# Optimization experiments

Hardware: AMD Instinct MI355X
Metric: run time of the kernel (lower is better)

Reference implementation:

```python
import jax, jax.numpy as jnp
import numpy as np

D_MODEL = 1024
HEADS = 16
HEAD_DIM = D_MODEL // HEADS


def setup_inputs() -> dict:
    key = jax.random.key(0)
    ks = jax.random.split(key, 11)
    B, S = 2, 2048
    scale = 1.0 / np.sqrt(D_MODEL)
    inp = {
        "Q": jax.random.normal(ks[0], (B, S, D_MODEL), jnp.float32),
        "K": jax.random.normal(ks[1], (B, S, D_MODEL), jnp.float32),
        "V": jax.random.normal(ks[2], (B, S, D_MODEL), jnp.float32),
        "Wq": jax.random.normal(ks[3], (D_MODEL, D_MODEL), jnp.float32) * scale,
        "bq": jnp.zeros((D_MODEL,), jnp.float32),
        "Wk": jax.random.normal(ks[4], (D_MODEL, D_MODEL), jnp.float32) * scale,
        "bk": jnp.zeros((D_MODEL,), jnp.float32),
        "Wv": jax.random.normal(ks[5], (D_MODEL, D_MODEL), jnp.float32) * scale,
        "bv": jnp.zeros((D_MODEL,), jnp.float32),
        "Wo": jax.random.normal(ks[6], (D_MODEL, D_MODEL), jnp.float32) * scale,
        "bo": jnp.zeros((D_MODEL,), jnp.float32),
    }
    return inp


def reference(Q, K, V, Wq, bq, Wk, bk, Wv, bv, Wo, bo):
    B, S, _ = Q.shape
    # Linear projections (nn.Linear: x @ W^T + b), split into heads: [B, H, S, Dh]
    def proj(x, W, b):
        y = x @ W.T + b
        return y.reshape(B, S, HEADS, HEAD_DIM).transpose(0, 2, 1, 3)

    q = proj(Q, Wq, bq)
    k = proj(K, Wk, bk)
    v = proj(V, Wv, bv)

    # Scaled dot-product attention (dropout is identity in eval / p=0)
    scores = jnp.einsum("bhqd,bhkd->bhqk", q, k) / jnp.sqrt(
        jnp.asarray(HEAD_DIM, q.dtype)
    )
    weights = jax.nn.softmax(scores, axis=-1)
    ctx = jnp.einsum("bhqk,bhkd->bhqd", weights, v)  # [B, H, S, Dh]

    # Concatenate heads and output projection
    concat = ctx.transpose(0, 2, 1, 3).reshape(B, S, D_MODEL)
    return concat @ Wo.T + bo
```

## Files before the change

kernel.cpp:

```cpp
#include <hip/hip_runtime.h>
#include <hip/hip_bf16.h>

#define D_MODEL 1024
#define HEADS 16
#define HDIM 64
#define BATCH 2
#define SEQ 2048
#define MROWS (BATCH*SEQ)

typedef __attribute__((ext_vector_type(8))) short bf16x8;
typedef __attribute__((ext_vector_type(4))) float f32x4;
typedef __attribute__((ext_vector_type(16))) float f32x16;
typedef __attribute__((ext_vector_type(4))) float float4v;
typedef __attribute__((ext_vector_type(4))) unsigned u32x4;
typedef __attribute__((ext_vector_type(4))) short s16x4;

typedef const __attribute__((address_space(1))) void gconst_t;
typedef __attribute__((address_space(3))) void lds_t;
#define GLD16(g, l) __builtin_amdgcn_global_load_lds((gconst_t*)(g), (lds_t*)(l), 16, 0, 0)

#if __has_builtin(__builtin_amdgcn_exp2f)
#define EXP2(x) __builtin_amdgcn_exp2f(x)
#else
#define EXP2(x) __builtin_exp2f(x)
#endif

__device__ __forceinline__ unsigned short f2b(float f) {
  unsigned u = __builtin_bit_cast(unsigned, f);
  u += 0x7fffu + ((u >> 16) & 1u);
  return (unsigned short)(u >> 16);
}

__device__ __forceinline__ unsigned cvtpk(float lo, float hi) {
  unsigned r;
  asm volatile("v_cvt_pk_bf16_f32 %0, %1, %2" : "=v"(r) : "v"(lo), "v"(hi));
  return r;
}

__global__ __launch_bounds__(256)
void cast_all(const float* __restrict__ Q, const float* __restrict__ K,
              const float* __restrict__ V, const float* __restrict__ Wq,
              const float* __restrict__ Wk, const float* __restrict__ Wv,
              const float* __restrict__ Wo, char* __restrict__ ws)
{
  const size_t MB = 1024*1024;
  int b = blockIdx.x;
  const float* src; short* dst; int rb;
  if (b < 6144) {
    int t = b >> 11; rb = b & 2047;
    src = (t == 0) ? Q : (t == 1) ? K : V;
    dst = (short*)(ws + (size_t)t*8*MB);
  } else {
    int t = (b - 6144) >> 9; rb = (b - 6144) & 511;
    src = (t == 0) ? Wq : (t == 1) ? Wk : (t == 2) ? Wv : Wo;
    dst = (short*)(ws + (24 + 2*(size_t)t)*MB);
  }
  int i = rb*256 + threadIdx.x;
  const float4v* s = (const float4v*)src;
  float4v a = s[2*(size_t)i], c = s[2*(size_t)i + 1];
  bf16x8 o;
  o[0] = (short)f2b(a[0]); o[1] = (short)f2b(a[1]);
  o[2] = (short)f2b(a[2]); o[3] = (short)f2b(a[3]);
  o[4] = (short)f2b(c[0]); o[5] = (short)f2b(c[1]);
  o[6] = (short)f2b(c[2]); o[7] = (short)f2b(c[3]);
  *(bf16x8*)(dst + 8*(size_t)i) = o;
}

__global__ __launch_bounds__(256)
void gemm_qkv(const short* __restrict__ Qb, const short* __restrict__ Kb,
              const short* __restrict__ Vb, const short* __restrict__ Wqb,
              const short* __restrict__ Wkb, const short* __restrict__ Wvb,
              const float* __restrict__ bq, const float* __restrict__ bk,
              const float* __restrict__ bv, short* __restrict__ qp,
              short* __restrict__ kp, short* __restrict__ vp)
{
  __shared__ __align__(16) char smemc[65536];
  short* const lA0 = (short*)smemc;
  short* const lA1 = (short*)(smemc + 16384);
  short* const lB0 = (short*)(smemc + 32768);
  short* const lB1 = (short*)(smemc + 49152);
  short* const lT  = (short*)smemc;

  const int z = blockIdx.z;
  const short* A = (z == 0) ? Qb : (z == 1) ? Kb : Vb;
  const short* W = (z == 0) ? Wqb : (z == 1) ? Wkb : Wvb;
  const float* bias = (z == 0) ? bq : (z == 1) ? bk : bv;

  const int tid  = threadIdx.x;
  const int wid  = tid >> 6;
  const int lane = tid & 63;
  const int bm = blockIdx.x, bn = blockIdx.y;
  const int wr = wid >> 1, wc = wid & 1;

  f32x4 acc[4][4] = {};

  const int srow = tid >> 3;
  const int cswz = (((tid & 7) * 16) ^ ((srow & 7) << 4)) >> 1;
  const short* gA = A + (size_t)(bm*128 + srow)*D_MODEL + cswz;
  const short* gB = W + (size_t)(bn*128 + srow)*D_MODEL + cswz;

#define QKV_STAGE(kt, bA, bB) do { \
    const int ko_ = (kt)*64; \
    GLD16(gA + ko_,              (bA) + (     wid*8)*64); \
    GLD16(gA + 32*D_MODEL + ko_, (bA) + (32 + wid*8)*64); \
    GLD16(gA + 64*D_MODEL + ko_, (bA) + (64 + wid*8)*64); \
    GLD16(gA + 96*D_MODEL + ko_, (bA) + (96 + wid*8)*64); \
    GLD16(gB + ko_,              (bB) + (     wid*8)*64); \
    GLD16(gB + 32*D_MODEL + ko_, (bB) + (32 + wid*8)*64); \
    GLD16(gB + 64*D_MODEL + ko_, (bB) + (64 + wid*8)*64); \
    GLD16(gB + 96*D_MODEL + ko_, (bB) + (96 + wid*8)*64); \
  } while (0)

  const int fro = lane & 15;
  const int xr7 = (fro & 7) << 4;
  const int c0  = ((((lane >> 4) << 4))      ^ xr7) >> 1;
  const int c1  = ((64 + ((lane >> 4) << 4)) ^ xr7) >> 1;

  QKV_STAGE(0, lA0, lB0);
  __syncthreads();

  for (int kt = 0; kt < D_MODEL/64; ++kt) {
    const int cur = kt & 1;
    if (kt + 1 < D_MODEL/64)
      QKV_STAGE(kt + 1, cur ? lA0 : lA1, cur ? lB0 : lB1);
    const short* LA = cur ? lA1 : lA0;
    const short* LB = cur ? lB1 : lB0;
    #pragma unroll
    for (int ks2 = 0; ks2 < 2; ++ks2) {
      const int cc = ks2 ? c1 : c0;
      bf16x8 af[4], bfv[4];
      #pragma unroll
      for (int i = 0; i < 4; ++i)
        af[i] = *(const bf16x8*)&LA[(wr*64 + i*16 + fro)*64 + cc];
      #pragma unroll
      for (int j = 0; j < 4; ++j)
        bfv[j] = *(const bf16x8*)&LB[(wc*64 + j*16 + fro)*64 + cc];
      #pragma unroll
      for (int i = 0; i < 4; ++i)
        #pragma unroll
        for (int j = 0; j < 4; ++j)
          acc[i][j] = __builtin_amdgcn_mfma_f32_16x16x32_bf16(af[i], bfv[j], acc[i][j], 0, 0, 0);
    }
    __syncthreads();
  }
#undef QKV_STAGE

  if (z < 2) {
    const float sc = (z == 0) ? 0.125f*1.44269504f : 1.0f;
    short* out = (z == 0) ? qp : kp;
    #pragma unroll
    for (int i = 0; i < 4; ++i) {
      #pragma unroll
      for (int r = 0; r < 4; ++r) {
        const int m = bm*128 + wr*64 + i*16 + (lane>>4)*4 + r;
        const int b = m >> 11, s = m & (SEQ-1);
        #pragma unroll
        for (int j = 0; j < 4; ++j) {
          const int n = bn*128 + wc*64 + j*16 + fro;
          const int h = n >> 6, dh = n & 63;
          float v = (acc[i][j][r] + bias[n]) * sc;
          out[((size_t)(b*HEADS + h)*SEQ + s)*HDIM + dh] = (short)f2b(v);
        }
      }
    }
  } else {
    #pragma unroll
    for (int i = 0; i < 4; ++i) {
      #pragma unroll
      for (int r = 0; r < 4; ++r) {
        const int ml = wr*64 + i*16 + (lane>>4)*4 + r;
        #pragma unroll
        for (int j = 0; j < 4; ++j) {
          const int nl = wc*64 + j*16 + fro;
          lT[nl*129 + ml] = (short)f2b(acc[i][j][r] + bias[bn*128 + nl]);
        }
      }
    }
    __syncthreads();
    const int nl = tid >> 1, mh = (tid & 1) * 64;
    const int n = bn*128 + nl, h = n >> 6, dh = n & 63;
    const int b  = (bm*128) >> 11;
    const int s0 = (bm*128) & (SEQ-1);
    const size_t base = ((size_t)(b*HEADS + h)*HDIM + dh)*SEQ + s0 + mh;
    #pragma unroll
    for (int v8 = 0; v8 < 8; ++v8) {
      bf16x8 vv;
      #pragma unroll
      for (int e = 0; e < 8; ++e) vv[e] = lT[nl*129 + mh + v8*8 + e];
      *(bf16x8*)&vp[base + v8*8] = vv;
    }
  }
}

__global__ __launch_bounds__(256)
void gemm_out(const short* __restrict__ A, const short* __restrict__ W,
              const float* __restrict__ bias, float* __restrict__ out)
{
  __shared__ __align__(16) char smemc[65536];
  short* const lA0 = (short*)smemc;
  short* const lA1 = (short*)(smemc + 16384);
  short* const lB0 = (short*)(smemc + 32768);
  short* const lB1 = (short*)(smemc + 49152);

  const int tid  = threadIdx.x;
  const int wid  = tid >> 6;
  const int lane = tid & 63;
  const int bm = blockIdx.x, bn = blockIdx.y;
  const int wr = wid >> 1, wc = wid & 1;

  f32x4 acc[4][4] = {};
  const int srow = tid >> 3;
  const int cswz = (((tid & 7) * 16) ^ ((srow & 7) << 4)) >> 1;
  const short* gA = A + (size_t)(bm*128 + srow)*D_MODEL + cswz;
  const short* gB = W + (size_t)(bn*128 + srow)*D_MODEL + cswz;

#define OUT_STAGE(kt, bA, bB) do { \
    const int ko_ = (kt)*64; \
    GLD16(gA + ko_,              (bA) + (     wid*8)*64); \
    GLD16(gA + 32*D_MODEL + ko_, (bA) + (32 + wid*8)*64); \
    GLD16(gA + 64*D_MODEL + ko_, (bA) + (64 + wid*8)*64); \
    GLD16(gA + 96*D_MODEL + ko_, (bA) + (96 + wid*8)*64); \
    GLD16(gB + ko_,              (bB) + (     wid*8)*64); \
    GLD16(gB + 32*D_MODEL + ko_, (bB) + (32 + wid*8)*64); \
    GLD16(gB + 64*D_MODEL + ko_, (bB) + (64 + wid*8)*64); \
    GLD16(gB + 96*D_MODEL + ko_, (bB) + (96 + wid*8)*64); \
  } while (0)

  const int fro = lane & 15;
  const int xr7 = (fro & 7) << 4;
  const int c0  = ((((lane >> 4) << 4))      ^ xr7) >> 1;
  const int c1  = ((64 + ((lane >> 4) << 4)) ^ xr7) >> 1;

  OUT_STAGE(0, lA0, lB0);
  __syncthreads();

  for (int kt = 0; kt < D_MODEL/64; ++kt) {
    const int cur = kt & 1;
    if (kt + 1 < D_MODEL/64)
      OUT_STAGE(kt + 1, cur ? lA0 : lA1, cur ? lB0 : lB1);
    const short* LA = cur ? lA1 : lA0;
    const short* LB = cur ? lB1 : lB0;
    #pragma unroll
    for (int ks2 = 0; ks2 < 2; ++ks2) {
      const int cc = ks2 ? c1 : c0;
      bf16x8 af[4], bfv[4];
      #pragma unroll
      for (int i = 0; i < 4; ++i)
        af[i] = *(const bf16x8*)&LA[(wr*64 + i*16 + fro)*64 + cc];
      #pragma unroll
      for (int j = 0; j < 4; ++j)
        bfv[j] = *(const bf16x8*)&LB[(wc*64 + j*16 + fro)*64 + cc];
      #pragma unroll
      for (int i = 0; i < 4; ++i)
        #pragma unroll
        for (int j = 0; j < 4; ++j)
          acc[i][j] = __builtin_amdgcn_mfma_f32_16x16x32_bf16(af[i], bfv[j], acc[i][j], 0, 0, 0);
    }
    __syncthreads();
  }
#undef OUT_STAGE

  #pragma unroll
  for (int i = 0; i < 4; ++i) {
    #pragma unroll
    for (int r = 0; r < 4; ++r) {
      const int m = bm*128 + wr*64 + i*16 + (lane>>4)*4 + r;
      #pragma unroll
      for (int j = 0; j < 4; ++j) {
        const int n = bn*128 + wc*64 + j*16 + fro;
        out[(size_t)m*D_MODEL + n] = acc[i][j][r] + bias[n];
      }
    }
  }
}

__global__ __launch_bounds__(512)
void attn(const short* __restrict__ qws, const short* __restrict__ kws,
          const short* __restrict__ vws, short* __restrict__ ctx)
{
  __shared__ __align__(16) short lK[2][2][64*64];
  __shared__ __align__(16) short lV[2][2][64*64];

  const int tid = threadIdx.x, wid = tid >> 6, lane = tid & 63;
  const int sw = wid & 3, half = wid >> 2;
  const int bid = blockIdx.x;
  const int wg = (bid & 7) * 64 + (bid >> 3);
  const int qt = wg & 15, bh = wg >> 4;
  const size_t hb = (size_t)bh * SEQ * HDIM;

  const int lane31 = lane & 31, hi = lane >> 5;
  const int tidl = sw*64 + lane;
  const int tr0  = tidl >> 3;
  const int cswz = (((tidl & 7) * 16) ^ ((tr0 & 7) << 4)) >> 1;

  const short* gK = kws + hb;
  const short* gV = vws + hb;

#define STAGEKV(t, bb) do { \
    GLD16(gK + (size_t)((t)*64 + tr0)*HDIM + cswz,      &lK[half][bb][(sw*8)*64]); \
    GLD16(gK + (size_t)((t)*64 + 32 + tr0)*HDIM + cswz, &lK[half][bb][(32+sw*8)*64]); \
    GLD16(gV + (size_t)tr0*SEQ + (t)*64 + cswz,         &lV[half][bb][(sw*8)*64]); \
    GLD16(gV + (size_t)(32+tr0)*SEQ + (t)*64 + cswz,    &lV[half][bb][(32+sw*8)*64]); \
  } while (0)

  const int kt0 = half * 16;
  STAGEKV(kt0, 0);

  const int q = qt*128 + sw*32 + lane31;
  const short* gq = qws + hb + (size_t)q*HDIM + hi*8;
  bf16x8 qf[4];
  #pragma unroll
  for (int ks = 0; ks < 4; ++ks) qf[ks] = *(const bf16x8*)(gq + ks*16);

  f32x16 o0 = {}, o1 = {};
  float lrow = 0.f;
  const int swz = (lane31 & 7) << 4;

  __syncthreads();

  for (int k2 = 0; k2 < 16; ++k2) {
    const short* Kc = &lK[half][k2 & 1][0];
    const short* Vc = &lV[half][k2 & 1][0];
    if (k2 + 1 < 16) STAGEKV(kt0 + k2 + 1, (k2 + 1) & 1);

    #pragma unroll
    for (int kb = 0; kb < 2; ++kb) {
      f32x16 s = {};
      __builtin_amdgcn_s_setprio(1);
      #pragma unroll
      for (int ks = 0; ks < 4; ++ks) {
        bf16x8 kf = *(const bf16x8*)&Kc[(kb*32 + lane31)*64 + (((ks*32 + hi*16) ^ swz) >> 1)];
        s = __builtin_amdgcn_mfma_f32_32x32x16_bf16(kf, qf[ks], s, 0, 0, 0);
      }
      __builtin_amdgcn_s_setprio(0);

      float p[16]; float rs = 0.f;
      #pragma unroll
      for (int r = 0; r < 16; ++r) { p[r] = EXP2(s[r]); rs += p[r]; }
      lrow += rs;

      unsigned w0 = cvtpk(p[0],  p[1]),  w1 = cvtpk(p[2],  p[3]);
      unsigned w2 = cvtpk(p[4],  p[5]),  w3 = cvtpk(p[6],  p[7]);
      unsigned w4 = cvtpk(p[8],  p[9]),  w5 = cvtpk(p[10], p[11]);
      unsigned w6 = cvtpk(p[12], p[13]), w7 = cvtpk(p[14], p[15]);
      unsigned y0 = hi ? w0 : w2, y1 = hi ? w1 : w3;
      unsigned y2 = hi ? w4 : w6, y3 = hi ? w5 : w7;
      unsigned z0 = (unsigned)__shfl_xor((int)y0, 32);
      unsigned z1 = (unsigned)__shfl_xor((int)y1, 32);
      unsigned z2 = (unsigned)__shfl_xor((int)y2, 32);
      unsigned z3 = (unsigned)__shfl_xor((int)y3, 32);
      u32x4 pw0 = { hi ? z0 : w0, hi ? z1 : w1, hi ? w2 : z0, hi ? w3 : z1 };
      u32x4 pw1 = { hi ? z2 : w4, hi ? z3 : w5, hi ? w6 : z2, hi ? w7 : z3 };
      bf16x8 pa0 = __builtin_bit_cast(bf16x8, pw0);
      bf16x8 pa1 = __builtin_bit_cast(bf16x8, pw1);

      __builtin_amdgcn_s_setprio(1);
      #pragma unroll
      for (int ksl = 0; ksl < 2; ++ksl) {
        const int vcol = ((kb*64 + ksl*32 + hi*16) ^ swz) >> 1;
        bf16x8 pav = ksl ? pa1 : pa0;
        bf16x8 vf0 = *(const bf16x8*)&Vc[lane31*64 + vcol];
        bf16x8 vf1 = *(const bf16x8*)&Vc[(32 + lane31)*64 + vcol];
        o0 = __builtin_amdgcn_mfma_f32_32x32x16_bf16(vf0, pav, o0, 0, 0, 0);
        o1 = __builtin_amdgcn_mfma_f32_32x32x16_bf16(vf1, pav, o1, 0, 0, 0);
      }
      __builtin_amdgcn_s_setprio(0);
    }
    __syncthreads();
  }

  lrow += __shfl_xor(lrow, 32);

  float* xo = (float*)&lK[0][0][0];
  float* xl = (float*)&lV[0][0][0];
  if (half == 1) {
    #pragma unroll
    for (int g = 0; g < 4; ++g) {
      #pragma unroll
      for (int e = 0; e < 4; ++e) {
        const int dh = g*8 + hi*4 + e;
        xo[sw*2048 + dh*32 + lane31]        = o0[g*4 + e];
        xo[sw*2048 + (32 + dh)*32 + lane31] = o1[g*4 + e];
      }
    }
    if (hi == 0) xl[sw*32 + lane31] = lrow;
  }
  __syncthreads();
  if (half == 0) {
    const float inv = 1.0f / (lrow + xl[sw*32 + lane31]);
    const int b_ = bh >> 4, h_ = bh & (HEADS-1);
    const size_t base = ((size_t)(b_*SEQ) + q)*D_MODEL + h_*HDIM;
    #pragma unroll
    for (int g = 0; g < 4; ++g) {
      s16x4 pk0, pk1;
      #pragma unroll
      for (int e = 0; e < 4; ++e) {
        const int dh = g*8 + hi*4 + e;
        pk0[e] = (short)f2b((o0[g*4+e] + xo[sw*2048 + dh*32 + lane31]) * inv);
        pk1[e] = (short)f2b((o1[g*4+e] + xo[sw*2048 + (32+dh)*32 + lane31]) * inv);
      }
      *(s16x4*)&ctx[base +      g*8 + hi*4] = pk0;
      *(s16x4*)&ctx[base + 32 + g*8 + hi*4] = pk1;
    }
  }
#undef STAGEKV
}

extern "C" void kernel_launch(void* const* d_in, const int* in_sizes, int n_in,
                              void* d_out, int out_size, void* d_ws, size_t ws_size,
                              hipStream_t stream)
{
  const float* Q  = (const float*)d_in[0];
  const float* K  = (const float*)d_in[1];
  const float* V  = (const float*)d_in[2];
  const float* Wq = (const float*)d_in[3];
  const float* bq = (const float*)d_in[4];
  const float* Wk = (const float*)d_in[5];
  const float* bk = (const float*)d_in[6];
  const float* Wv = (const float*)d_in[7];
  const float* bv = (const float*)d_in[8];
  const float* Wo = (const float*)d_in[9];
  const float* bo = (const float*)d_in[10];

  char* ws = (char*)d_ws;
  const size_t MB = 1024*1024;
  short* Qb  = (short*)(ws +  0*MB);
  short* Kb  = (short*)(ws +  8*MB);
  short* Vb  = (short*)(ws + 16*MB);
  short* Wqb = (short*)(ws + 24*MB);
  short* Wkb = (short*)(ws + 26*MB);
  short* Wvb = (short*)(ws + 28*MB);
  short* Wob = (short*)(ws + 30*MB);
  short* qp  = (short*)(ws + 32*MB);
  short* kp  = (short*)(ws + 40*MB);
  short* vp  = (short*)(ws + 48*MB);
  short* cx  = (short*)(ws + 56*MB);

  cast_all<<<8192, 256, 0, stream>>>(Q, K, V, Wq, Wk, Wv, Wo, ws);
  gemm_qkv<<<dim3(MROWS/128, D_MODEL/128, 3), 256, 0, stream>>>(
      Qb, Kb, Vb, Wqb, Wkb, Wvb, bq, bk, bv, qp, kp, vp);
  attn<<<512, 512, 0, stream>>>(qp, kp, vp, cx);
  gemm_out<<<dim3(MROWS/128, D_MODEL/128), 256, 0, stream>>>(cx, Wob, bo, (float*)d_out);
}
```

Before: 118.8 us.

## Fuse fp32-to-bf16 cast into GEMM tile loads, drop separate cast kernel

Removes the standalone cast_all kernel and has gemm_qkv and gemm_out read fp32 inputs and weights directly. Each thread loads them into registers, converts with v_cvt_pk_bf16_f32, and writes the swizzled bf16 tile to LDS after the MFMA loop, giving register-staged double buffering. This cuts a kernel launch and the write-then-reread of the bf16 copies. In exchange the GEMMs read twice as many bytes per tile, re-read each weight fp32 tile from many blocks, and use more registers.

```diff
diff --git a/kernel.cpp b/kernel.cpp
--- a/kernel.cpp
+++ b/kernel.cpp
@@ -37,39 +37,16 @@
   return r;
 }
 
+__device__ __forceinline__ bf16x8 cvt8(float4v lo, float4v hi) {
+  u32x4 u = { cvtpk(lo[0], lo[1]), cvtpk(lo[2], lo[3]),
+              cvtpk(hi[0], hi[1]), cvtpk(hi[2], hi[3]) };
+  return __builtin_bit_cast(bf16x8, u);
+}
+
 __global__ __launch_bounds__(256)
-void cast_all(const float* __restrict__ Q, const float* __restrict__ K,
-              const float* __restrict__ V, const float* __restrict__ Wq,
-              const float* __restrict__ Wk, const float* __restrict__ Wv,
-              const float* __restrict__ Wo, char* __restrict__ ws)
-{
-  const size_t MB = 1024*1024;
-  int b = blockIdx.x;
-  const float* src; short* dst; int rb;
-  if (b < 6144) {
-    int t = b >> 11; rb = b & 2047;
-    src = (t == 0) ? Q : (t == 1) ? K : V;
-    dst = (short*)(ws + (size_t)t*8*MB);
-  } else {
-    int t = (b - 6144) >> 9; rb = (b - 6144) & 511;
-    src = (t == 0) ? Wq : (t == 1) ? Wk : (t == 2) ? Wv : Wo;
-    dst = (short*)(ws + (24 + 2*(size_t)t)*MB);
-  }
-  int i = rb*256 + threadIdx.x;
-  const float4v* s = (const float4v*)src;
-  float4v a = s[2*(size_t)i], c = s[2*(size_t)i + 1];
-  bf16x8 o;
-  o[0] = (short)f2b(a[0]); o[1] = (short)f2b(a[1]);
-  o[2] = (short)f2b(a[2]); o[3] = (short)f2b(a[3]);
-  o[4] = (short)f2b(c[0]); o[5] = (short)f2b(c[1]);
-  o[6] = (short)f2b(c[2]); o[7] = (short)f2b(c[3]);
-  *(bf16x8*)(dst + 8*(size_t)i) = o;
-}
-
-__global__ __launch_bounds__(256)
-void gemm_qkv(const short* __restrict__ Qb, const short* __restrict__ Kb,
-              const short* __restrict__ Vb, const short* __restrict__ Wqb,
-              const short* __restrict__ Wkb, const short* __restrict__ Wvb,
+void gemm_qkv(const float* __restrict__ Qf, const float* __restrict__ Kf,
+              const float* __restrict__ Vf, const float* __restrict__ Wqf,
+              const float* __restrict__ Wkf, const float* __restrict__ Wvf,
               const float* __restrict__ bq, const float* __restrict__ bk,
               const float* __restrict__ bv, short* __restrict__ qp,
               short* __restrict__ kp, short* __restrict__ vp)
@@ -82,8 +59,8 @@
   short* const lT  = (short*)smemc;
 
   const int z = blockIdx.z;
-  const short* A = (z == 0) ? Qb : (z == 1) ? Kb : Vb;
-  const short* W = (z == 0) ? Wqb : (z == 1) ? Wkb : Wvb;
+  const float* A = (z == 0) ? Qf : (z == 1) ? Kf : Vf;
+  const float* W = (z == 0) ? Wqf : (z == 1) ? Wkf : Wvf;
   const float* bias = (z == 0) ? bq : (z == 1) ? bk : bv;
 
   const int tid  = threadIdx.x;
@@ -95,34 +72,40 @@
   f32x4 acc[4][4] = {};
 
   const int srow = tid >> 3;
-  const int cswz = (((tid & 7) * 16) ^ ((srow & 7) << 4)) >> 1;
-  const short* gA = A + (size_t)(bm*128 + srow)*D_MODEL + cswz;
-  const short* gB = W + (size_t)(bn*128 + srow)*D_MODEL + cswz;
-
-#define QKV_STAGE(kt, bA, bB) do { \
-    const int ko_ = (kt)*64; \
-    GLD16(gA + ko_,              (bA) + (     wid*8)*64); \
-    GLD16(gA + 32*D_MODEL + ko_, (bA) + (32 + wid*8)*64); \
-    GLD16(gA + 64*D_MODEL + ko_, (bA) + (64 + wid*8)*64); \
-    GLD16(gA + 96*D_MODEL + ko_, (bA) + (96 + wid*8)*64); \
-    GLD16(gB + ko_,              (bB) + (     wid*8)*64); \
-    GLD16(gB + 32*D_MODEL + ko_, (bB) + (32 + wid*8)*64); \
-    GLD16(gB + 64*D_MODEL + ko_, (bB) + (64 + wid*8)*64); \
-    GLD16(gB + 96*D_MODEL + ko_, (bB) + (96 + wid*8)*64); \
-  } while (0)
+  const int gseg = (tid & 7) * 8;
+  const int dso  = ((((tid & 7) * 16) ^ ((srow & 7) << 4)) >> 1);
+  const float* gA = A + (size_t)(bm*128 + srow)*D_MODEL + gseg;
+  const float* gB = W + (size_t)(bn*128 + srow)*D_MODEL + gseg;
+
+  float4v sa[8], sb[8];
+#define QKV_LOAD(kt_) do { \
+    const int ko_ = (kt_)*64; \
+    _Pragma("unroll") \
+    for (int r_ = 0; r_ < 4; ++r_) { \
+      sa[2*r_]   = *(const float4v*)(gA + (size_t)r_*32*D_MODEL + ko_); \
+      sa[2*r_+1] = *(const float4v*)(gA + (size_t)r_*32*D_MODEL + ko_ + 4); \
+      sb[2*r_]   = *(const float4v*)(gB + (size_t)r_*32*D_MODEL + ko_); \
+      sb[2*r_+1] = *(const float4v*)(gB + (size_t)r_*32*D_MODEL + ko_ + 4); \
+    } } while (0)
+#define QKV_WRITE(bA_, bB_) do { \
+    _Pragma("unroll") \
+    for (int r_ = 0; r_ < 4; ++r_) { \
+      *(bf16x8*)&(bA_)[(32*r_ + srow)*64 + dso] = cvt8(sa[2*r_], sa[2*r_+1]); \
+      *(bf16x8*)&(bB_)[(32*r_ + srow)*64 + dso] = cvt8(sb[2*r_], sb[2*r_+1]); \
+    } } while (0)
 
   const int fro = lane & 15;
   const int xr7 = (fro & 7) << 4;
   const int c0  = ((((lane >> 4) << 4))      ^ xr7) >> 1;
   const int c1  = ((64 + ((lane >> 4) << 4)) ^ xr7) >> 1;
 
-  QKV_STAGE(0, lA0, lB0);
+  QKV_LOAD(0);
+  QKV_WRITE(lA0, lB0);
   __syncthreads();
 
   for (int kt = 0; kt < D_MODEL/64; ++kt) {
     const int cur = kt & 1;
-    if (kt + 1 < D_MODEL/64)
-      QKV_STAGE(kt + 1, cur ? lA0 : lA1, cur ? lB0 : lB1);
+    if (kt + 1 < D_MODEL/64) QKV_LOAD(kt + 1);
     const short* LA = cur ? lA1 : lA0;
     const short* LB = cur ? lB1 : lB0;
     #pragma unroll
@@ -141,9 +124,12 @@
         for (int j = 0; j < 4; ++j)
           acc[i][j] = __builtin_amdgcn_mfma_f32_16x16x32_bf16(af[i], bfv[j], acc[i][j], 0, 0, 0);
     }
+    if (kt + 1 < D_MODEL/64)
+      QKV_WRITE(cur ? lA0 : lA1, cur ? lB0 : lB1);
     __syncthreads();
   }
-#undef QKV_STAGE
+#undef QKV_LOAD
+#undef QKV_WRITE
 
   if (z < 2) {
     const float sc = (z == 0) ? 0.125f*1.44269504f : 1.0f;
@@ -193,7 +179,7 @@
 }
 
 __global__ __launch_bounds__(256)
-void gemm_out(const short* __restrict__ A, const short* __restrict__ W,
+void gemm_out(const short* __restrict__ A, const float* __restrict__ W,
               const float* __restrict__ bias, float* __restrict__ out)
 {
   __shared__ __align__(16) char smemc[65536];
@@ -210,20 +196,31 @@
 
   f32x4 acc[4][4] = {};
   const int srow = tid >> 3;
-  const int cswz = (((tid & 7) * 16) ^ ((srow & 7) << 4)) >> 1;
+  const int gseg = (tid & 7) * 8;
+  const int dso  = ((((tid & 7) * 16) ^ ((srow & 7) << 4)) >> 1);
+  const int cswz = dso;
   const short* gA = A + (size_t)(bm*128 + srow)*D_MODEL + cswz;
-  const short* gB = W + (size_t)(bn*128 + srow)*D_MODEL + cswz;
-
-#define OUT_STAGE(kt, bA, bB) do { \
-    const int ko_ = (kt)*64; \
-    GLD16(gA + ko_,              (bA) + (     wid*8)*64); \
-    GLD16(gA + 32*D_MODEL + ko_, (bA) + (32 + wid*8)*64); \
-    GLD16(gA + 64*D_MODEL + ko_, (bA) + (64 + wid*8)*64); \
-    GLD16(gA + 96*D_MODEL + ko_, (bA) + (96 + wid*8)*64); \
-    GLD16(gB + ko_,              (bB) + (     wid*8)*64); \
-    GLD16(gB + 32*D_MODEL + ko_, (bB) + (32 + wid*8)*64); \
-    GLD16(gB + 64*D_MODEL + ko_, (bB) + (64 + wid*8)*64); \
-    GLD16(gB + 96*D_MODEL + ko_, (bB) + (96 + wid*8)*64); \
+  const float* gB = W + (size_t)(bn*128 + srow)*D_MODEL + gseg;
+
+  float4v sb[8];
+#define OUT_LOADB(kt_) do { \
+    const int ko_ = (kt_)*64; \
+    _Pragma("unroll") \
+    for (int r_ = 0; r_ < 4; ++r_) { \
+      sb[2*r_]   = *(const float4v*)(gB + (size_t)r_*32*D_MODEL + ko_); \
+      sb[2*r_+1] = *(const float4v*)(gB + (size_t)r_*32*D_MODEL + ko_ + 4); \
+    } } while (0)
+#define OUT_WRITEB(bB_) do { \
+    _Pragma("unroll") \
+    for (int r_ = 0; r_ < 4; ++r_) \
+      *(bf16x8*)&(bB_)[(32*r_ + srow)*64 + dso] = cvt8(sb[2*r_], sb[2*r_+1]); \
+    } while (0)
+#define OUT_STAGEA(kt_, bA_) do { \
+    const int ko_ = (kt_)*64; \
+    GLD16(gA + ko_,              (bA_) + (     wid*8)*64); \
+    GLD16(gA + 32*D_MODEL + ko_, (bA_) + (32 + wid*8)*64); \
+    GLD16(gA + 64*D_MODEL + ko_, (bA_) + (64 + wid*8)*64); \
+    GLD16(gA + 96*D_MODEL + ko_, (bA_) + (96 + wid*8)*64); \
   } while (0)
 
   const int fro = lane & 15;
@@ -231,13 +228,17 @@
   const int c0  = ((((lane >> 4) << 4))      ^ xr7) >> 1;
   const int c1  = ((64 + ((lane >> 4) << 4)) ^ xr7) >> 1;
 
-  OUT_STAGE(0, lA0, lB0);
+  OUT_LOADB(0);
+  OUT_STAGEA(0, lA0);
+  OUT_WRITEB(lB0);
   __syncthreads();
 
   for (int kt = 0; kt < D_MODEL/64; ++kt) {
     const int cur = kt & 1;
-    if (kt + 1 < D_MODEL/64)
-      OUT_STAGE(kt + 1, cur ? lA0 : lA1, cur ? lB0 : lB1);
+    if (kt + 1 < D_MODEL/64) {
+      OUT_LOADB(kt + 1);
+      OUT_STAGEA(kt + 1, cur ? lA0 : lA1);
+    }
     const short* LA = cur ? lA1 : lA0;
     const short* LB = cur ? lB1 : lB0;
     #pragma unroll
@@ -256,9 +257,13 @@
         for (int j = 0; j < 4; ++j)
           acc[i][j] = __builtin_amdgcn_mfma_f32_16x16x32_bf16(af[i], bfv[j], acc[i][j], 0, 0, 0);
     }
+    if (kt + 1 < D_MODEL/64)
+      OUT_WRITEB(cur ? lB0 : lB1);
     __syncthreads();
   }
-#undef OUT_STAGE
+#undef OUT_LOADB
+#undef OUT_WRITEB
+#undef OUT_STAGEA
 
   #pragma unroll
   for (int i = 0; i < 4; ++i) {
@@ -424,21 +429,13 @@
 
   char* ws = (char*)d_ws;
   const size_t MB = 1024*1024;
-  short* Qb  = (short*)(ws +  0*MB);
-  short* Kb  = (short*)(ws +  8*MB);
-  short* Vb  = (short*)(ws + 16*MB);
-  short* Wqb = (short*)(ws + 24*MB);
-  short* Wkb = (short*)(ws + 26*MB);
-  short* Wvb = (short*)(ws + 28*MB);
-  short* Wob = (short*)(ws + 30*MB);
   short* qp  = (short*)(ws + 32*MB);
   short* kp  = (short*)(ws + 40*MB);
   short* vp  = (short*)(ws + 48*MB);
   short* cx  = (short*)(ws + 56*MB);
 
-  cast_all<<<8192, 256, 0, stream>>>(Q, K, V, Wq, Wk, Wv, Wo, ws);
   gemm_qkv<<<dim3(MROWS/128, D_MODEL/128, 3), 256, 0, stream>>>(
-      Qb, Kb, Vb, Wqb, Wkb, Wvb, bq, bk, bv, qp, kp, vp);
+      Q, K, V, Wq, Wk, Wv, bq, bk, bv, qp, kp, vp);
   attn<<<512, 512, 0, stream>>>(qp, kp, vp, cx);
-  gemm_out<<<dim3(MROWS/128, D_MODEL/128), 256, 0, stream>>>(cx, Wob, bo, (float*)d_out);
-}
+  gemm_out<<<dim3(MROWS/128, D_MODEL/128), 256, 0, stream>>>(cx, Wo, bo, (float*)d_out);
+}
```

Measured after the change: 124.7 us. 1.05x slower.

## Process two 32-query tiles per wave in attention, halving block size

Applied to the files above, without the earlier changes.

Each attention wave now handles 64 queries (two 32-row sub-tiles) instead of 32, so every K and V fragment read from LDS feeds two MFMAs. The block shrinks from 8 to 4 waves, and K/V staging is restructured so each wave issues 8 global-to-LDS loads instead of 4. This cuts LDS read traffic per FLOP and raises MFMA density per wave. In exchange it doubles accumulator and Q registers, which may reduce occupancy or cause spills, and leaves fewer waves to hide latency.

```diff
diff --git a/kernel.cpp b/kernel.cpp
--- a/kernel.cpp
+++ b/kernel.cpp
@@ -274,7 +274,7 @@
   }
 }
 
-__global__ __launch_bounds__(512)
+__global__ __launch_bounds__(256)
 void attn(const short* __restrict__ qws, const short* __restrict__ kws,
           const short* __restrict__ vws, short* __restrict__ ctx)
 {
@@ -282,38 +282,43 @@
   __shared__ __align__(16) short lV[2][2][64*64];
 
   const int tid = threadIdx.x, wid = tid >> 6, lane = tid & 63;
-  const int sw = wid & 3, half = wid >> 2;
+  const int half = wid >> 1, sq = wid & 1;
   const int bid = blockIdx.x;
   const int wg = (bid & 7) * 64 + (bid >> 3);
   const int qt = wg & 15, bh = wg >> 4;
   const size_t hb = (size_t)bh * SEQ * HDIM;
 
   const int lane31 = lane & 31, hi = lane >> 5;
-  const int tidl = sw*64 + lane;
-  const int tr0  = tidl >> 3;
-  const int cswz = (((tidl & 7) * 16) ^ ((tr0 & 7) << 4)) >> 1;
+  const int grp = lane >> 3, gran = lane & 7;
+  const int cswz = ((gran * 16) ^ (grp << 4)) >> 1;
 
   const short* gK = kws + hb;
   const short* gV = vws + hb;
 
 #define STAGEKV(t, bb) do { \
-    GLD16(gK + (size_t)((t)*64 + tr0)*HDIM + cswz,      &lK[half][bb][(sw*8)*64]); \
-    GLD16(gK + (size_t)((t)*64 + 32 + tr0)*HDIM + cswz, &lK[half][bb][(32+sw*8)*64]); \
-    GLD16(gV + (size_t)tr0*SEQ + (t)*64 + cswz,         &lV[half][bb][(sw*8)*64]); \
-    GLD16(gV + (size_t)(32+tr0)*SEQ + (t)*64 + cswz,    &lV[half][bb][(32+sw*8)*64]); \
-  } while (0)
+    _Pragma("unroll") \
+    for (int c_ = 0; c_ < 4; ++c_) { \
+      GLD16(gK + (size_t)((t)*64 + c_*16 + sq*8 + grp)*HDIM + cswz, \
+            &lK[half][bb][(c_*16 + sq*8)*64]); \
+      GLD16(gV + (size_t)(c_*16 + sq*8 + grp)*SEQ + (t)*64 + cswz, \
+            &lV[half][bb][(c_*16 + sq*8)*64]); \
+    } } while (0)
 
   const int kt0 = half * 16;
   STAGEKV(kt0, 0);
 
-  const int q = qt*128 + sw*32 + lane31;
-  const short* gq = qws + hb + (size_t)q*HDIM + hi*8;
-  bf16x8 qf[4];
+  const int q0 = qt*128 + sq*64 + lane31;
+  const short* gq0 = qws + hb + (size_t)q0*HDIM + hi*8;
+  bf16x8 qa[4], qb[4];
   #pragma unroll
-  for (int ks = 0; ks < 4; ++ks) qf[ks] = *(const bf16x8*)(gq + ks*16);
-
-  f32x16 o0 = {}, o1 = {};
-  float lrow = 0.f;
+  for (int ks = 0; ks < 4; ++ks) {
+    qa[ks] = *(const bf16x8*)(gq0 + ks*16);
+    qb[ks] = *(const bf16x8*)(gq0 + 32*HDIM + ks*16);
+  }
+
+  f32x16 oa0 = {}, oa1 = {};
+  f32x16 ob0 = {}, ob1 = {};
+  float la = 0.f, lb = 0.f;
   const int swz = (lane31 & 7) << 4;
 
   __syncthreads();
@@ -325,20 +330,20 @@
 
     #pragma unroll
     for (int kb = 0; kb < 2; ++kb) {
-      f32x16 s = {};
+      f32x16 s0 = {}, s1 = {};
       __builtin_amdgcn_s_setprio(1);
       #pragma unroll
       for (int ks = 0; ks < 4; ++ks) {
         bf16x8 kf = *(const bf16x8*)&Kc[(kb*32 + lane31)*64 + (((ks*32 + hi*16) ^ swz) >> 1)];
-        s = __builtin_amdgcn_mfma_f32_32x32x16_bf16(kf, qf[ks], s, 0, 0, 0);
+        s0 = __builtin_amdgcn_mfma_f32_32x32x16_bf16(kf, qa[ks], s0, 0, 0, 0);
+        s1 = __builtin_amdgcn_mfma_f32_32x32x16_bf16(kf, qb[ks], s1, 0, 0, 0);
       }
       __builtin_amdgcn_s_setprio(0);
 
       float p[16]; float rs = 0.f;
       #pragma unroll
-      for (int r = 0; r < 16; ++r) { p[r] = EXP2(s[r]); rs += p[r]; }
-      lrow += rs;
-
+      for (int r = 0; r < 16; ++r) { p[r] = EXP2(s0[r]); rs += p[r]; }
+      la += rs;
       unsigned w0 = cvtpk(p[0],  p[1]),  w1 = cvtpk(p[2],  p[3]);
       unsigned w2 = cvtpk(p[4],  p[5]),  w3 = cvtpk(p[6],  p[7]);
       unsigned w4 = cvtpk(p[8],  p[9]),  w5 = cvtpk(p[10], p[11]);
@@ -351,56 +356,94 @@
       unsigned z3 = (unsigned)__shfl_xor((int)y3, 32);
       u32x4 pw0 = { hi ? z0 : w0, hi ? z1 : w1, hi ? w2 : z0, hi ? w3 : z1 };
       u32x4 pw1 = { hi ? z2 : w4, hi ? z3 : w5, hi ? w6 : z2, hi ? w7 : z3 };
-      bf16x8 pa0 = __builtin_bit_cast(bf16x8, pw0);
-      bf16x8 pa1 = __builtin_bit_cast(bf16x8, pw1);
+      bf16x8 paA0 = __builtin_bit_cast(bf16x8, pw0);
+      bf16x8 paA1 = __builtin_bit_cast(bf16x8, pw1);
+
+      #pragma unroll
+      for (int r = 0; r < 16; ++r) p[r] = EXP2(s1[r]);
+      rs = 0.f;
+      #pragma unroll
+      for (int r = 0; r < 16; ++r) rs += p[r];
+      lb += rs;
+      w0 = cvtpk(p[0],  p[1]);  w1 = cvtpk(p[2],  p[3]);
+      w2 = cvtpk(p[4],  p[5]);  w3 = cvtpk(p[6],  p[7]);
+      w4 = cvtpk(p[8],  p[9]);  w5 = cvtpk(p[10], p[11]);
+      w6 = cvtpk(p[12], p[13]); w7 = cvtpk(p[14], p[15]);
+      y0 = hi ? w0 : w2; y1 = hi ? w1 : w3;
+      y2 = hi ? w4 : w6; y3 = hi ? w5 : w7;
+      z0 = (unsigned)__shfl_xor((int)y0, 32);
+      z1 = (unsigned)__shfl_xor((int)y1, 32);
+      z2 = (unsigned)__shfl_xor((int)y2, 32);
+      z3 = (unsigned)__shfl_xor((int)y3, 32);
+      u32x4 pw2 = { hi ? z0 : w0, hi ? z1 : w1, hi ? w2 : z0, hi ? w3 : z1 };
+      u32x4 pw3 = { hi ? z2 : w4, hi ? z3 : w5, hi ? w6 : z2, hi ? w7 : z3 };
+      bf16x8 paB0 = __builtin_bit_cast(bf16x8, pw2);
+      bf16x8 paB1 = __builtin_bit_cast(bf16x8, pw3);
 
       __builtin_amdgcn_s_setprio(1);
       #pragma unroll
       for (int ksl = 0; ksl < 2; ++ksl) {
         const int vcol = ((kb*64 + ksl*32 + hi*16) ^ swz) >> 1;
-        bf16x8 pav = ksl ? pa1 : pa0;
+        bf16x8 pavA = ksl ? paA1 : paA0;
+        bf16x8 pavB = ksl ? paB1 : paB0;
         bf16x8 vf0 = *(const bf16x8*)&Vc[lane31*64 + vcol];
         bf16x8 vf1 = *(const bf16x8*)&Vc[(32 + lane31)*64 + vcol];
-        o0 = __builtin_amdgcn_mfma_f32_32x32x16_bf16(vf0, pav, o0, 0, 0, 0);
-        o1 = __builtin_amdgcn_mfma_f32_32x32x16_bf16(vf1, pav, o1, 0, 0, 0);
+        oa0 = __builtin_amdgcn_mfma_f32_32x32x16_bf16(vf0, pavA, oa0, 0, 0, 0);
+        oa1 = __builtin_amdgcn_mfma_f32_32x32x16_bf16(vf1, pavA, oa1, 0, 0, 0);
+        ob0 = __builtin_amdgcn_mfma_f32_32x32x16_bf16(vf0, pavB, ob0, 0, 0, 0);
+        ob1 = __builtin_amdgcn_mfma_f32_32x32x16_bf16(vf1, pavB, ob1, 0, 0, 0);
       }
       __builtin_amdgcn_s_setprio(0);
     }
     __syncthreads();
   }
 
-  lrow += __shfl_xor(lrow, 32);
+  la += __shfl_xor(la, 32);
+  lb += __shfl_xor(lb, 32);
 
   float* xo = (float*)&lK[0][0][0];
   float* xl = (float*)&lV[0][0][0];
   if (half == 1) {
+    const int bA = (sq*2 + 0)*2048, bB = (sq*2 + 1)*2048;
     #pragma unroll
     for (int g = 0; g < 4; ++g) {
       #pragma unroll
       for (int e = 0; e < 4; ++e) {
         const int dh = g*8 + hi*4 + e;
-        xo[sw*2048 + dh*32 + lane31]        = o0[g*4 + e];
-        xo[sw*2048 + (32 + dh)*32 + lane31] = o1[g*4 + e];
-      }
-    }
-    if (hi == 0) xl[sw*32 + lane31] = lrow;
+        xo[bA + dh*32 + lane31]        = oa0[g*4 + e];
+        xo[bA + (32 + dh)*32 + lane31] = oa1[g*4 + e];
+        xo[bB + dh*32 + lane31]        = ob0[g*4 + e];
+        xo[bB + (32 + dh)*32 + lane31] = ob1[g*4 + e];
+      }
+    }
+    if (hi == 0) {
+      xl[(sq*2 + 0)*32 + lane31] = la;
+      xl[(sq*2 + 1)*32 + lane31] = lb;
+    }
   }
   __syncthreads();
   if (half == 0) {
-    const float inv = 1.0f / (lrow + xl[sw*32 + lane31]);
     const int b_ = bh >> 4, h_ = bh & (HEADS-1);
-    const size_t base = ((size_t)(b_*SEQ) + q)*D_MODEL + h_*HDIM;
+    const float invA = 1.0f / (la + xl[(sq*2 + 0)*32 + lane31]);
+    const float invB = 1.0f / (lb + xl[(sq*2 + 1)*32 + lane31]);
+    const int bA = (sq*2 + 0)*2048, bB = (sq*2 + 1)*2048;
+    const size_t baseA = ((size_t)(b_*SEQ) + q0)*D_MODEL + h_*HDIM;
+    const size_t baseB = baseA + (size_t)32*D_MODEL;
     #pragma unroll
     for (int g = 0; g < 4; ++g) {
-      s16x4 pk0, pk1;
+      s16x4 a0, a1, b0v, b1v;
       #pragma unroll
       for (int e = 0; e < 4; ++e) {
         const int dh = g*8 + hi*4 + e;
-        pk0[e] = (short)f2b((o0[g*4+e] + xo[sw*2048 + dh*32 + lane31]) * inv);
-        pk1[e] = (short)f2b((o1[g*4+e] + xo[sw*2048 + (32+dh)*32 + lane31]) * inv);
-      }
-      *(s16x4*)&ctx[base +      g*8 + hi*4] = pk0;
-      *(s16x4*)&ctx[base + 32 + g*8 + hi*4] = pk1;
+        a0[e]  = (short)f2b((oa0[g*4+e] + xo[bA + dh*32 + lane31]) * invA);
+        a1[e]  = (short)f2b((oa1[g*4+e] + xo[bA + (32+dh)*32 + lane31]) * invA);
+        b0v[e] = (short)f2b((ob0[g*4+e] + xo[bB + dh*32 + lane31]) * invB);
+        b1v[e] = (short)f2b((ob1[g*4+e] + xo[bB + (32+dh)*32 + lane31]) * invB);
+      }
+      *(s16x4*)&ctx[baseA +      g*8 + hi*4] = a0;
+      *(s16x4*)&ctx[baseA + 32 + g*8 + hi*4] = a1;
+      *(s16x4*)&ctx[baseB +      g*8 + hi*4] = b0v;
+      *(s16x4*)&ctx[baseB + 32 + g*8 + hi*4] = b1v;
     }
   }
 #undef STAGEKV
@@ -439,6 +482,6 @@
   cast_all<<<8192, 256, 0, stream>>>(Q, K, V, Wq, Wk, Wv, Wo, ws);
   gemm_qkv<<<dim3(MROWS/128, D_MODEL/128, 3), 256, 0, stream>>>(
       Qb, Kb, Vb, Wqb, Wkb, Wvb, bq, bk, bv, qp, kp, vp);
-  attn<<<512, 512, 0, stream>>>(qp, kp, vp, cx);
+  attn<<<512, 256, 0, stream>>>(qp, kp, vp, cx);
   gemm_out<<<dim3(MROWS/128, D_MODEL/128), 256, 0, stream>>>(cx, Wob, bo, (float*)d_out);
 }
```

New measurement: 127.4 us. 7.3% more time.
